# Performance work log

Hardware: AMD Instinct MI355X
Metric: run time of the kernel (lower is better)

## Reference

```python
import jax, jax.numpy as jnp
import numpy as np

EPS = 1e-12  # F.normalize default eps


def _l2norm(x, axis):
    n = jnp.sqrt(jnp.sum(x * x, axis=axis, keepdims=True))
    return x / jnp.maximum(n, EPS)


def setup_inputs() -> dict:
    key = jax.random.key(0)
    k1, k2, k3, k4 = jax.random.split(key, 4)
    N, T, C, K = 64, 577, 768, 64
    return {
        "grids": jax.random.normal(k1, (N, T, C), dtype=jnp.float32),
        "conv_w": jax.random.normal(k2, (K, C), dtype=jnp.float32) * 0.03,
        "conv_b": jax.random.normal(k3, (K,), dtype=jnp.float32) * 0.01,
        "centroids": jax.random.normal(k4, (K, C), dtype=jnp.float32) * 0.03,
    }


def reference(grids, conv_w, conv_b, centroids):
    # grids: (N, 577, 768) -> (N, C=768, T=577), matching view+permute in torch
    N = grids.shape[0]
    x = jnp.transpose(grids.reshape(N, 577, 768), (0, 2, 1))  # (N, C, T)
    # per-token L2 normalization over channel dim
    x = _l2norm(x, axis=1)
    # 1x1 conv == per-token linear: (N, K, T)
    logits = jnp.einsum('kc,nct->nkt', conv_w, x) + conv_b[None, :, None]
    a = jax.nn.softmax(logits, axis=1)  # softmax over regions K
    # NetVLAD algebraic rewrite of sum_t a[n,k,t]*(x[n,:,t]-c[k,:]):
    #   = (a @ x^T)[n,k,c] - sum_t(a)[n,k] * c[k,c]
    p = jnp.einsum('nkt,nct->nkc', a, x) - a.sum(axis=-1)[:, :, None] * centroids[None]
    p = _l2norm(p, axis=2)             # intra-region normalization
    p = p.reshape(N, -1)               # (N, K*C)
    p = _l2norm(p, axis=1)             # global normalization
    return p
```

## Files before the change

kernel.cpp:

```cpp
#include <hip/hip_runtime.h>
#include <math.h>

#define TT 577
#define TP 640
#define CCH 768
#define KR 64
#define NB 64

typedef __attribute__((ext_vector_type(8))) short bf16x8;
typedef __attribute__((ext_vector_type(8))) unsigned short ushort8;
typedef __attribute__((ext_vector_type(4))) float f32x4;

static constexpr float EPSF = 1e-12f;

static __device__ inline unsigned short f2bf(float f) {
    union { float f; unsigned int u; } v; v.f = f;
    return (unsigned short)((v.u + 0x7FFFu + ((v.u >> 16) & 1u)) >> 16);
}
static __device__ inline float bf2f(unsigned short b) {
    union { unsigned int u; float f; } v; v.u = ((unsigned int)b) << 16;
    return v.f;
}

__global__ __launch_bounds__(256) void k_logits(
    const float* __restrict__ grids,
    const float* __restrict__ conv_w,
    const float* __restrict__ conv_b,
    unsigned short* __restrict__ ws_a,
    float* __restrict__ ws_norm)
{
    __shared__ __align__(16) unsigned short Wl[2][KR * 136];

    const int tid  = threadIdx.x;
    const int lane = tid & 63;
    const int w    = tid >> 6;
    const int n    = blockIdx.x / 10;
    const int tb   = (blockIdx.x - n * 10) << 6;
    const int t0w  = tb + (w << 4);

    const int lr = lane & 15;
    const int lg = lane >> 4;

    const int tokA = t0w + lr;
    const bool validA = (tokA < TT);
    const float* gsrc = grids + ((size_t)n * TT + tokA) * CCH + (lg << 3);

    float4 wreg[4][2];
    auto load_w = [&](int c0) {
        #pragma unroll
        for (int it = 0; it < 4; ++it) {
            int f = tid + (it << 8);
            int kr = f >> 4, c8 = (f & 15) << 3;
            const float* src = conv_w + (size_t)kr * CCH + c0 + c8;
            wreg[it][0] = *reinterpret_cast<const float4*>(src);
            wreg[it][1] = *reinterpret_cast<const float4*>(src + 4);
        }
    };
    auto store_w = [&](int buf) {
        #pragma unroll
        for (int it = 0; it < 4; ++it) {
            int f = tid + (it << 8);
            int kr = f >> 4, c8 = (f & 15) << 3;
            ushort8 o;
            o[0] = f2bf(wreg[it][0].x); o[1] = f2bf(wreg[it][0].y);
            o[2] = f2bf(wreg[it][0].z); o[3] = f2bf(wreg[it][0].w);
            o[4] = f2bf(wreg[it][1].x); o[5] = f2bf(wreg[it][1].y);
            o[6] = f2bf(wreg[it][1].z); o[7] = f2bf(wreg[it][1].w);
            *reinterpret_cast<ushort8*>(&Wl[buf][kr * 136 + c8]) = o;
        }
    };

    f32x4 acc[4] = {};
    float ss = 0.f;

    load_w(0);
    store_w(0);
    __syncthreads();

    for (int ch = 0; ch < 6; ++ch) {
        if (ch < 5) {
            load_w((ch + 1) << 7);
            store_w((ch + 1) & 1);
        }
        const int c0 = ch << 7;
        const unsigned short* Wb = Wl[ch & 1];

        #pragma unroll
        for (int s = 0; s < 4; ++s) {
            float a8[8];
            if (validA) {
                float4 u0 = *reinterpret_cast<const float4*>(gsrc + c0 + (s << 5));
                float4 u1 = *reinterpret_cast<const float4*>(gsrc + c0 + (s << 5) + 4);
                a8[0]=u0.x; a8[1]=u0.y; a8[2]=u0.z; a8[3]=u0.w;
                a8[4]=u1.x; a8[5]=u1.y; a8[6]=u1.z; a8[7]=u1.w;
            } else {
                #pragma unroll
                for (int j = 0; j < 8; ++j) a8[j] = 0.f;
            }
            bf16x8 afrag;
            #pragma unroll
            for (int j = 0; j < 8; ++j) {
                ss = fmaf(a8[j], a8[j], ss);
                ((unsigned short*)&afrag)[j] = f2bf(a8[j]);
            }
            const int cl = (s << 5) + (lg << 3);
            #pragma unroll
            for (int rt = 0; rt < 4; ++rt) {
                bf16x8 bfrag = *reinterpret_cast<const bf16x8*>(&Wb[(rt*16 + lr)*136 + cl]);
                acc[rt] = __builtin_amdgcn_mfma_f32_16x16x32_bf16(afrag, bfrag, acc[rt], 0, 0, 0);
            }
        }
        __syncthreads();
    }

    ss += __shfl_xor(ss, 16);
    ss += __shfl_xor(ss, 32);
    const float nrm = sqrtf(ss);
    const float inv = 1.0f / fmaxf(nrm, EPSF);
    if (lane < 16) ws_norm[n * TP + t0w + lane] = nrm;

    float b_[4];
    #pragma unroll
    for (int rt = 0; rt < 4; ++rt) b_[rt] = conv_b[rt*16 + lr];

    float invT[4];
    #pragma unroll
    for (int reg = 0; reg < 4; ++reg) invT[reg] = __shfl(inv, (lg << 2) + reg);

    float lgt[4][4], mx[4];
    #pragma unroll
    for (int reg = 0; reg < 4; ++reg) {
        float m = -1e30f;
        #pragma unroll
        for (int rt = 0; rt < 4; ++rt) {
            lgt[rt][reg] = fmaf(acc[rt][reg], invT[reg], b_[rt]);
            m = fmaxf(m, lgt[rt][reg]);
        }
        mx[reg] = m;
    }
    #pragma unroll
    for (int msk = 1; msk < 16; msk <<= 1) {
        #pragma unroll
        for (int reg = 0; reg < 4; ++reg) mx[reg] = fmaxf(mx[reg], __shfl_xor(mx[reg], msk));
    }
    float ex[4][4], sm[4] = {0.f, 0.f, 0.f, 0.f};
    #pragma unroll
    for (int rt = 0; rt < 4; ++rt) {
        #pragma unroll
        for (int reg = 0; reg < 4; ++reg) {
            ex[rt][reg] = __expf(lgt[rt][reg] - mx[reg]);
            sm[reg] += ex[rt][reg];
        }
    }
    #pragma unroll
    for (int msk = 1; msk < 16; msk <<= 1) {
        #pragma unroll
        for (int reg = 0; reg < 4; ++reg) sm[reg] += __shfl_xor(sm[reg], msk);
    }

    unsigned short* Abuf = &Wl[0][0] + (size_t)w * KR * 24;
    #pragma unroll
    for (int reg = 0; reg < 4; ++reg) {
        const int trow = (lg << 2) + reg;
        const bool vt = (t0w + trow) < TT;
        const float scale = vt ? (invT[reg] / sm[reg]) : 0.f;
        #pragma unroll
        for (int rt = 0; rt < 4; ++rt)
            Abuf[(rt*16 + lr)*24 + trow] = f2bf(ex[rt][reg] * scale);
    }
    __syncthreads();

    {
        ushort8 r0 = *reinterpret_cast<const ushort8*>(&Abuf[lane * 24]);
        ushort8 r1 = *reinterpret_cast<const ushort8*>(&Abuf[lane * 24 + 8]);
        unsigned short* dst = ws_a + ((size_t)n * KR + lane) * TP + t0w;
        *reinterpret_cast<ushort8*>(dst)     = r0;
        *reinterpret_cast<ushort8*>(dst + 8) = r1;
    }
}

__global__ __launch_bounds__(256) void k_vlad(
    const float* __restrict__ grids,
    const unsigned short* __restrict__ ws_a,
    const float* __restrict__ ws_norm,
    const float* __restrict__ centroids,
    float* __restrict__ out)
{
    __shared__ float asum_red[4][64];
    __shared__ float asum_s[64];

    const int tid  = threadIdx.x;
    const int lane = tid & 63;
    const int w    = tid >> 6;
    const int n    = blockIdx.x / 12;
    const int c0   = (blockIdx.x - n * 12) << 6;
    const int lr   = lane & 15;
    const int lg   = lane >> 4;

    {
        const int kr = tid & 63, q = tid >> 6;
        const unsigned short* ap = ws_a + ((size_t)n * KR + kr) * TP;
        const float* np = ws_norm + n * TP;
        float s = 0.f;
        for (int t = q * 8; t < TP; t += 32) {
            ushort8 av = *reinterpret_cast<const ushort8*>(ap + t);
            float4 n0 = *reinterpret_cast<const float4*>(np + t);
            float4 n1 = *reinterpret_cast<const float4*>(np + t + 4);
            s += bf2f(av[0])*n0.x + bf2f(av[1])*n0.y + bf2f(av[2])*n0.z + bf2f(av[3])*n0.w
               + bf2f(av[4])*n1.x + bf2f(av[5])*n1.y + bf2f(av[6])*n1.z + bf2f(av[7])*n1.w;
        }
        asum_red[q][kr] = s;
    }
    __syncthreads();
    if (tid < 64)
        asum_s[tid] = asum_red[0][tid] + asum_red[1][tid] + asum_red[2][tid] + asum_red[3][tid];
    __syncthreads();

    const int c = c0 + (w << 4) + lr;
    const unsigned short* abase = ws_a + ((size_t)n * KR + lr) * TP + (lg << 3);
    const float* gb = grids + (size_t)n * TT * CCH + c;

    auto load_frags = [&](int t0, bf16x8* af, bf16x8& bfv) {
        #pragma unroll
        for (int rt = 0; rt < 4; ++rt)
            af[rt] = *reinterpret_cast<const bf16x8*>(abase + (size_t)rt * 16 * TP + t0);
        const int tb2 = t0 + (lg << 3);
        if (t0 + 32 <= TT) {
            #pragma unroll
            for (int j = 0; j < 8; ++j)
                ((unsigned short*)&bfv)[j] = f2bf(gb[(size_t)(tb2 + j) * CCH]);
        } else {
            #pragma unroll
            for (int j = 0; j < 8; ++j) {
                float v = (tb2 + j < TT) ? gb[(size_t)(tb2 + j) * CCH] : 0.f;
                ((unsigned short*)&bfv)[j] = f2bf(v);
            }
        }
    };

    f32x4 acc[4] = {};
    bf16x8 afA[4], afB[4];
    bf16x8 bfA, bfB;

    load_frags(0, afA, bfA);
    #pragma unroll 2
    for (int t0 = 0; t0 < TT; t0 += 64) {
        if (t0 + 32 < TT) load_frags(t0 + 32, afB, bfB);
        #pragma unroll
        for (int rt = 0; rt < 4; ++rt)
            acc[rt] = __builtin_amdgcn_mfma_f32_16x16x32_bf16(afA[rt], bfA, acc[rt], 0, 0, 0);
        if (t0 + 32 >= TT) break;
        if (t0 + 64 < TT) load_frags(t0 + 64, afA, bfA);
        #pragma unroll
        for (int rt = 0; rt < 4; ++rt)
            acc[rt] = __builtin_amdgcn_mfma_f32_16x16x32_bf16(afB[rt], bfB, acc[rt], 0, 0, 0);
    }

    #pragma unroll
    for (int rt = 0; rt < 4; ++rt) {
        #pragma unroll
        for (int reg = 0; reg < 4; ++reg) {
            const int kr = rt * 16 + (lg << 2) + reg;
            out[((size_t)n * KR + kr) * CCH + c] =
                acc[rt][reg] - asum_s[kr] * centroids[(size_t)kr * CCH + c];
        }
    }
}

__global__ __launch_bounds__(64) void kc_norm_kernel(float* __restrict__ out)
{
    float4* p = reinterpret_cast<float4*>(out) + (size_t)blockIdx.x * 192;
    const int l = threadIdx.x;
    float4 v0 = p[l];
    float4 v1 = p[l + 64];
    float4 v2 = p[l + 128];
    float ss = v0.x*v0.x + v0.y*v0.y + v0.z*v0.z + v0.w*v0.w
             + v1.x*v1.x + v1.y*v1.y + v1.z*v1.z + v1.w*v1.w
             + v2.x*v2.x + v2.y*v2.y + v2.z*v2.z + v2.w*v2.w;
    #pragma unroll
    for (int m = 1; m < 64; m <<= 1) ss += __shfl_xor(ss, m);
    const float sc = 0.125f / fmaxf(sqrtf(ss), EPSF);
    v0.x*=sc; v0.y*=sc; v0.z*=sc; v0.w*=sc;
    v1.x*=sc; v1.y*=sc; v1.z*=sc; v1.w*=sc;
    v2.x*=sc; v2.y*=sc; v2.z*=sc; v2.w*=sc;
    p[l] = v0;
    p[l + 64] = v1;
    p[l + 128] = v2;
}

extern "C" void kernel_launch(void* const* d_in, const int* in_sizes, int n_in,
                              void* d_out, int out_size, void* d_ws, size_t ws_size,
                              hipStream_t stream)
{
    const float* grids     = (const float*)d_in[0];
    const float* conv_w    = (const float*)d_in[1];
    const float* conv_b    = (const float*)d_in[2];
    const float* centroids = (const float*)d_in[3];
    float* out = (float*)d_out;

    unsigned short* ws_a = (unsigned short*)d_ws;
    float* ws_norm = (float*)((char*)d_ws + (size_t)NB * KR * TP * 2);

    hipLaunchKernelGGL(k_logits, dim3(NB * 10), dim3(256), 0, stream,
                       grids, conv_w, conv_b, ws_a, ws_norm);
    hipLaunchKernelGGL(k_vlad, dim3(NB * 12), dim3(256), 0, stream,
                       grids, ws_a, ws_norm, centroids, out);
    hipLaunchKernelGGL(kc_norm_kernel, dim3(NB * KR), dim3(64), 0, stream, out);
}
```

Before: 82.47 us.

## Compute per-block softmax sums in logits kernel; drop asum recompute in vlad

The logits kernel now reduces softmax probabilities over its 64 tokens per region and writes a partial sum per block, so the vlad kernel only adds 10 partials instead of re-reading the whole bf16 assignment matrix and norms. This removes a redundant pass over ws_a (done 12 times per batch item) and the ws_norm buffer. The vlad main loop is also rewritten with macros and scalar accumulators as a manual double buffer. The asum now comes from fp32 probabilities rather than bf16-rounded ones, which changes rounding slightly.

After: 73.18 us. 1.13x faster.

```diff
diff --git a/kernel.cpp b/kernel.cpp
--- a/kernel.cpp
+++ b/kernel.cpp
@@ -17,17 +17,13 @@
     union { float f; unsigned int u; } v; v.f = f;
     return (unsigned short)((v.u + 0x7FFFu + ((v.u >> 16) & 1u)) >> 16);
 }
-static __device__ inline float bf2f(unsigned short b) {
-    union { unsigned int u; float f; } v; v.u = ((unsigned int)b) << 16;
-    return v.f;
-}
 
 __global__ __launch_bounds__(256) void k_logits(
     const float* __restrict__ grids,
     const float* __restrict__ conv_w,
     const float* __restrict__ conv_b,
     unsigned short* __restrict__ ws_a,
-    float* __restrict__ ws_norm)
+    float* __restrict__ ws_asum)
 {
     __shared__ __align__(16) unsigned short Wl[2][KR * 136];
 
@@ -117,7 +113,6 @@
     ss += __shfl_xor(ss, 32);
     const float nrm = sqrtf(ss);
     const float inv = 1.0f / fmaxf(nrm, EPSF);
-    if (lane < 16) ws_norm[n * TP + t0w + lane] = nrm;
 
     float b_[4];
     #pragma unroll
@@ -158,17 +153,41 @@
         for (int reg = 0; reg < 4; ++reg) sm[reg] += __shfl_xor(sm[reg], msk);
     }
 
+    float rsm[4];
+    #pragma unroll
+    for (int reg = 0; reg < 4; ++reg) {
+        const bool vt = (t0w + (lg << 2) + reg) < TT;
+        rsm[reg] = vt ? (1.0f / sm[reg]) : 0.f;
+    }
+
+    float pa[4];
+    #pragma unroll
+    for (int rt = 0; rt < 4; ++rt) {
+        pa[rt] = ex[rt][0]*rsm[0] + ex[rt][1]*rsm[1] + ex[rt][2]*rsm[2] + ex[rt][3]*rsm[3];
+        pa[rt] += __shfl_xor(pa[rt], 16);
+        pa[rt] += __shfl_xor(pa[rt], 32);
+    }
+    float* asum_lds = reinterpret_cast<float*>(&Wl[1][0]);
+    if (lane < 16) {
+        #pragma unroll
+        for (int rt = 0; rt < 4; ++rt)
+            asum_lds[(w << 6) + rt*16 + lane] = pa[rt];
+    }
+
     unsigned short* Abuf = &Wl[0][0] + (size_t)w * KR * 24;
     #pragma unroll
     for (int reg = 0; reg < 4; ++reg) {
         const int trow = (lg << 2) + reg;
-        const bool vt = (t0w + trow) < TT;
-        const float scale = vt ? (invT[reg] / sm[reg]) : 0.f;
+        const float scale = invT[reg] * rsm[reg];
         #pragma unroll
         for (int rt = 0; rt < 4; ++rt)
             Abuf[(rt*16 + lr)*24 + trow] = f2bf(ex[rt][reg] * scale);
     }
     __syncthreads();
+
+    if (tid < 64)
+        ws_asum[(size_t)blockIdx.x * 64 + tid] =
+            asum_lds[tid] + asum_lds[64 + tid] + asum_lds[128 + tid] + asum_lds[192 + tid];
 
     {
         ushort8 r0 = *reinterpret_cast<const ushort8*>(&Abuf[lane * 24]);
@@ -179,14 +198,33 @@
     }
 }
 
+#define LOADA(d0,d1,d2,d3,t0_)                                                   \
+    d0 = *reinterpret_cast<const bf16x8*>(abase +            (size_t)(t0_));     \
+    d1 = *reinterpret_cast<const bf16x8*>(abase + 16*TP +    (size_t)(t0_));     \
+    d2 = *reinterpret_cast<const bf16x8*>(abase + 32*TP +    (size_t)(t0_));     \
+    d3 = *reinterpret_cast<const bf16x8*>(abase + 48*TP +    (size_t)(t0_));
+
+#define LOADB(d,t0_) do {                                                        \
+    const int tb2_ = (t0_) + (lg << 3);                                          \
+    if ((t0_) + 32 <= TT) {                                                      \
+        _Pragma("unroll")                                                        \
+        for (int j_ = 0; j_ < 8; ++j_)                                           \
+            ((unsigned short*)&(d))[j_] = f2bf(gb[(size_t)(tb2_ + j_) * CCH]);   \
+    } else {                                                                     \
+        _Pragma("unroll")                                                        \
+        for (int j_ = 0; j_ < 8; ++j_) {                                         \
+            float v_ = (tb2_ + j_ < TT) ? gb[(size_t)(tb2_ + j_) * CCH] : 0.f;   \
+            ((unsigned short*)&(d))[j_] = f2bf(v_);                              \
+        }                                                                        \
+    } } while (0)
+
 __global__ __launch_bounds__(256) void k_vlad(
     const float* __restrict__ grids,
     const unsigned short* __restrict__ ws_a,
-    const float* __restrict__ ws_norm,
+    const float* __restrict__ ws_asum,
     const float* __restrict__ centroids,
     float* __restrict__ out)
 {
-    __shared__ float asum_red[4][64];
     __shared__ float asum_s[64];
 
     const int tid  = threadIdx.x;
@@ -197,72 +235,68 @@
     const int lr   = lane & 15;
     const int lg   = lane >> 4;
 
-    {
-        const int kr = tid & 63, q = tid >> 6;
-        const unsigned short* ap = ws_a + ((size_t)n * KR + kr) * TP;
-        const float* np = ws_norm + n * TP;
+    if (tid < 64) {
         float s = 0.f;
-        for (int t = q * 8; t < TP; t += 32) {
-            ushort8 av = *reinterpret_cast<const ushort8*>(ap + t);
-            float4 n0 = *reinterpret_cast<const float4*>(np + t);
-            float4 n1 = *reinterpret_cast<const float4*>(np + t + 4);
-            s += bf2f(av[0])*n0.x + bf2f(av[1])*n0.y + bf2f(av[2])*n0.z + bf2f(av[3])*n0.w
-               + bf2f(av[4])*n1.x + bf2f(av[5])*n1.y + bf2f(av[6])*n1.z + bf2f(av[7])*n1.w;
-        }
-        asum_red[q][kr] = s;
-    }
-    __syncthreads();
-    if (tid < 64)
-        asum_s[tid] = asum_red[0][tid] + asum_red[1][tid] + asum_red[2][tid] + asum_red[3][tid];
+        #pragma unroll
+        for (int b = 0; b < 10; ++b)
+            s += ws_asum[((size_t)n * 10 + b) * 64 + tid];
+        asum_s[tid] = s;
+    }
     __syncthreads();
 
     const int c = c0 + (w << 4) + lr;
     const unsigned short* abase = ws_a + ((size_t)n * KR + lr) * TP + (lg << 3);
     const float* gb = grids + (size_t)n * TT * CCH + c;
 
-    auto load_frags = [&](int t0, bf16x8* af, bf16x8& bfv) {
-        #pragma unroll
-        for (int rt = 0; rt < 4; ++rt)
-            af[rt] = *reinterpret_cast<const bf16x8*>(abase + (size_t)rt * 16 * TP + t0);
-        const int tb2 = t0 + (lg << 3);
-        if (t0 + 32 <= TT) {
-            #pragma unroll
-            for (int j = 0; j < 8; ++j)
-                ((unsigned short*)&bfv)[j] = f2bf(gb[(size_t)(tb2 + j) * CCH]);
-        } else {
-            #pragma unroll
-            for (int j = 0; j < 8; ++j) {
-                float v = (tb2 + j < TT) ? gb[(size_t)(tb2 + j) * CCH] : 0.f;
-                ((unsigned short*)&bfv)[j] = f2bf(v);
-            }
-        }
-    };
-
-    f32x4 acc[4] = {};
-    bf16x8 afA[4], afB[4];
-    bf16x8 bfA, bfB;
-
-    load_frags(0, afA, bfA);
-    #pragma unroll 2
-    for (int t0 = 0; t0 < TT; t0 += 64) {
-        if (t0 + 32 < TT) load_frags(t0 + 32, afB, bfB);
-        #pragma unroll
-        for (int rt = 0; rt < 4; ++rt)
-            acc[rt] = __builtin_amdgcn_mfma_f32_16x16x32_bf16(afA[rt], bfA, acc[rt], 0, 0, 0);
-        if (t0 + 32 >= TT) break;
-        if (t0 + 64 < TT) load_frags(t0 + 64, afA, bfA);
-        #pragma unroll
-        for (int rt = 0; rt < 4; ++rt)
-            acc[rt] = __builtin_amdgcn_mfma_f32_16x16x32_bf16(afB[rt], bfB, acc[rt], 0, 0, 0);
-    }
-
-    #pragma unroll
-    for (int rt = 0; rt < 4; ++rt) {
-        #pragma unroll
-        for (int reg = 0; reg < 4; ++reg) {
-            const int kr = rt * 16 + (lg << 2) + reg;
+    f32x4 acc0 = {}, acc1 = {}, acc2 = {}, acc3 = {};
+    bf16x8 a0, a1, a2, a3, b0;
+    bf16x8 p0, p1, p2, p3, q0;
+
+    LOADA(a0, a1, a2, a3, 0)
+    LOADB(b0, 0);
+
+    int t0 = 0;
+    while (true) {
+        int tn = t0 + 32;
+        if (tn < TT) { LOADA(p0, p1, p2, p3, tn) LOADB(q0, tn); }
+        acc0 = __builtin_amdgcn_mfma_f32_16x16x32_bf16(a0, b0, acc0, 0, 0, 0);
+        acc1 = __builtin_amdgcn_mfma_f32_16x16x32_bf16(a1, b0, acc1, 0, 0, 0);
+        acc2 = __builtin_amdgcn_mfma_f32_16x16x32_bf16(a2, b0, acc2, 0, 0, 0);
+        acc3 = __builtin_amdgcn_mfma_f32_16x16x32_bf16(a3, b0, acc3, 0, 0, 0);
+        t0 = tn;
+        if (t0 >= TT) break;
+
+        tn = t0 + 32;
+        if (tn < TT) { LOADA(a0, a1, a2, a3, tn) LOADB(b0, tn); }
+        acc0 = __builtin_amdgcn_mfma_f32_16x16x32_bf16(p0, q0, acc0, 0, 0, 0);
+        acc1 = __builtin_amdgcn_mfma_f32_16x16x32_bf16(p1, q0, acc1, 0, 0, 0);
+        acc2 = __builtin_amdgcn_mfma_f32_16x16x32_bf16(p2, q0, acc2, 0, 0, 0);
+        acc3 = __builtin_amdgcn_mfma_f32_16x16x32_bf16(p3, q0, acc3, 0, 0, 0);
+        t0 = tn;
+        if (t0 >= TT) break;
+    }
+
+    #pragma unroll
+    for (int reg = 0; reg < 4; ++reg) {
+        {
+            const int kr = 0*16 + (lg << 2) + reg;
             out[((size_t)n * KR + kr) * CCH + c] =
-                acc[rt][reg] - asum_s[kr] * centroids[(size_t)kr * CCH + c];
+                acc0[reg] - asum_s[kr] * centroids[(size_t)kr * CCH + c];
+        }
+        {
+            const int kr = 1*16 + (lg << 2) + reg;
+            out[((size_t)n * KR + kr) * CCH + c] =
+                acc1[reg] - asum_s[kr] * centroids[(size_t)kr * CCH + c];
+        }
+        {
+            const int kr = 2*16 + (lg << 2) + reg;
+            out[((size_t)n * KR + kr) * CCH + c] =
+                acc2[reg] - asum_s[kr] * centroids[(size_t)kr * CCH + c];
+        }
+        {
+            const int kr = 3*16 + (lg << 2) + reg;
+            out[((size_t)n * KR + kr) * CCH + c] =
+                acc3[reg] - asum_s[kr] * centroids[(size_t)kr * CCH + c];
         }
     }
 }
@@ -299,11 +333,11 @@
     float* out = (float*)d_out;
 
     unsigned short* ws_a = (unsigned short*)d_ws;
-    float* ws_norm = (float*)((char*)d_ws + (size_t)NB * KR * TP * 2);
+    float* ws_asum = (float*)((char*)d_ws + (size_t)NB * KR * TP * 2);
 
     hipLaunchKernelGGL(k_logits, dim3(NB * 10), dim3(256), 0, stream,
-                       grids, conv_w, conv_b, ws_a, ws_norm);
+                       grids, conv_w, conv_b, ws_a, ws_asum);
     hipLaunchKernelGGL(k_vlad, dim3(NB * 12), dim3(256), 0, stream,
-                       grids, ws_a, ws_norm, centroids, out);
+                       grids, ws_a, ws_asum, centroids, out);
     hipLaunchKernelGGL(kc_norm_kernel, dim3(NB * KR), dim3(64), 0, stream, out);
 }
```
